# Kernel tuning notes

Hardware: AMD Instinct MI355X
Metric: run time of the kernel (lower is better)

The kernel has to match this reference:

```python
import jax, jax.numpy as jnp
import numpy as np

B, N, R, E = 4, 50000, 100000, 1_600_000   # batch, nodes (wavelets_col), wavelets_row, nnz
D_IN, H1, H2, D_OUT = 32, 32, 16, 1
NEG_SLOPE = 0.2


def _xavier(k, shape):
    lim = float(np.sqrt(6.0 / (shape[0] + shape[1])))
    return jax.random.uniform(k, shape, jnp.float32, -lim, lim)


def setup_inputs() -> dict:
    key = jax.random.key(0)
    ks = jax.random.split(key, 16)
    # wavelets: sparse (R x N); inverse wavelets: sparse (N x R)
    w_rows = jax.random.randint(ks[0], (E,), 0, R)
    w_cols = jax.random.randint(ks[1], (E,), 0, N)
    wi_rows = jax.random.randint(ks[2], (E,), 0, N)
    wi_cols = jax.random.randint(ks[3], (E,), 0, R)
    return {
        "wavelets_indices": jnp.stack([w_rows, w_cols]),
        "wavelets_values": jax.random.normal(ks[4], (E,), jnp.float32) * 0.05,
        "wavelets_inverse_indices": jnp.stack([wi_rows, wi_cols]),
        "wavelets_inverse_values": jax.random.normal(ks[5], (E,), jnp.float32) * 0.05,
        "x_features": jax.random.normal(ks[6], (B, N, D_IN), jnp.float32),
        "W1": _xavier(ks[7], (D_IN, H1)),
        "diag1": 0.9 + 0.2 * jax.random.uniform(ks[8], (R,), jnp.float32),
        "W2": _xavier(ks[9], (H1, H2)),
        "diag2": 0.9 + 0.2 * jax.random.uniform(ks[10], (R,), jnp.float32),
        "reg_co_w": _xavier(ks[11], (H2, D_OUT)),
        "reg_co_b": jnp.zeros((D_OUT,), jnp.float32),
        "reg_co2_w": _xavier(ks[12], (H2, D_OUT)),
        "reg_co2_b": jnp.zeros((D_OUT,), jnp.float32),
    }


def _gw_layer(x, W, diag, w_idx, w_val, wi_idx, wi_val):
    # filtered = X @ W  -> (B, N, d)
    h = jnp.einsum("bnd,de->bne", x, W)
    d = W.shape[1]
    # T = wavelets (R x N) @ h  : scatter-add of gathered edge messages
    msg = h[:, w_idx[1], :] * w_val[None, :, None]          # (B, E, d)
    t = jnp.zeros((x.shape[0], R, d), h.dtype).at[:, w_idx[0], :].add(msg)
    # out = (wavelets_inverse * diag) (N x R) @ T  (diag rescales columns)
    coef = wi_val * diag[wi_idx[1]]                         # (E,)
    msg2 = t[:, wi_idx[1], :] * coef[None, :, None]         # (B, E, d)
    out = jnp.zeros((x.shape[0], N, d), h.dtype).at[:, wi_idx[0], :].add(msg2)
    return jax.nn.leaky_relu(out, NEG_SLOPE)                # dropout p=0.0 -> identity


def reference(wavelets_indices, wavelets_values, wavelets_inverse_indices,
              wavelets_inverse_values, x_features, W1, diag1, W2, diag2,
              reg_co_w, reg_co_b, reg_co2_w, reg_co2_b):
    x = _gw_layer(x_features, W1, diag1, wavelets_indices, wavelets_values,
                  wavelets_inverse_indices, wavelets_inverse_values)
    x = _gw_layer(x, W2, diag2, wavelets_indices, wavelets_values,
                  wavelets_inverse_indices, wavelets_inverse_values)
    co = x[:, -2, :] @ reg_co_w + reg_co_b                  # (B, 1)
    co2 = x[:, -1, :] @ reg_co2_w + reg_co2_b               # (B, 1)
    return jnp.concatenate([co[:, None, :], co2[:, None, :]], axis=1)  # (B, 2, 1)
```

## Files before the change

### kernel.cpp

```cpp
#include <hip/hip_runtime.h>

#define NEG_SLOPE 0.2f

static const int B = 4, N = 50000, R = 100000, E = 1600000;
static const int X2_CAP = 4096;
static const int R2_CAP = 4096;
static const int N1_CAP = 4096;
static const int WDEG  = 64;
static const int WIDEG = 96;
static const int I4PB = 512;


__global__ void fusedA(const float* __restrict__ x, const float* __restrict__ W1,
                       float* __restrict__ h1,
                       const int4* __restrict__ wi_rows4, const int* __restrict__ wi_cols,
                       const float* __restrict__ wi_val,
                       int* __restrict__ flagsR, int2* __restrict__ x2list,
                       int* __restrict__ x2tail, int* __restrict__ r2list,
                       int* __restrict__ r2tail, int e4, int G1) {
    if ((int)blockIdx.x < G1) {
        __shared__ float sW[32 * 32];
        for (int i = threadIdx.x; i < 1024; i += blockDim.x) sW[i] = W1[i];
        __syncthreads();
        int id = blockIdx.x * blockDim.x + threadIdx.x;
        if (id >= N * B) return;
        int n = id >> 2, b = id & 3;
        const float* xr = x + ((size_t)b * N + n) * 32;
        float acc[32];
#pragma unroll
        for (int c = 0; c < 32; ++c) acc[c] = 0.f;
#pragma unroll
        for (int k = 0; k < 32; ++k) {
            float xv = xr[k];
#pragma unroll
            for (int c = 0; c < 32; ++c) acc[c] += xv * sW[k * 32 + c];
        }
        float* o = h1 + ((size_t)n * B + b) * 32;
#pragma unroll
        for (int c = 0; c < 32; ++c) o[c] = acc[c];
    } else {
        int blk = blockIdx.x - G1;
        int base = blk * (blockDim.x * 4) + threadIdx.x;
#pragma unroll
        for (int k = 0; k < 4; ++k) {
            int i = base + k * blockDim.x;
            if (i >= e4) continue;
            int4 r = wi_rows4[i];
            int rr[4] = {r.x, r.y, r.z, r.w};
#pragma unroll
            for (int j = 0; j < 4; ++j) {
                if (rr[j] >= N - 2) {
                    int ed = i * 4 + j;
                    int col = wi_cols[ed];
                    int old = atomicOr(&flagsR[col], 1);
                    if (!(old & 1)) {
                        int p = atomicAdd(r2tail, 1);
                        if (p < R2_CAP) r2list[p] = col;
                    }
                    int pos = atomicAdd(x2tail, 1);
                    if (pos < X2_CAP)
                        x2list[pos] = make_int2(col * 2 + (rr[j] - (N - 2)),
                                                __float_as_int(wi_val[ed]));
                }
            }
        }
    }
}

__global__ void markB(const int4* __restrict__ w_rows4, const int* __restrict__ w_cols,
                      const int* __restrict__ flagsR, int* __restrict__ flagN1,
                      int* __restrict__ n1list, int* __restrict__ n1slot,
                      int* __restrict__ n1tail, int e4) {
    __shared__ int lcount, gbase;
    __shared__ int sbuf[2048];
    if (threadIdx.x == 0) lcount = 0;
    __syncthreads();
    int lane = threadIdx.x & 63;
#pragma unroll
    for (int k = 0; k < 2; ++k) {
        int i = blockIdx.x * I4PB + k * 256 + threadIdx.x;
        int4 r = make_int4(-1, -1, -1, -1);
        if (i < e4) r = w_rows4[i];
        int rr[4] = {r.x, r.y, r.z, r.w};
#pragma unroll
        for (int j = 0; j < 4; ++j) {
            bool isnew = false;
            int c = 0;
            if (rr[j] >= 0 && flagsR[rr[j]] != 0) {
                c = w_cols[i * 4 + j];
                int old = atomicOr(&flagN1[c], 1);
                isnew = (old == 0);
            }
            unsigned long long m = __ballot(isnew);
            if (m) {
                int leader = __ffsll(m) - 1;
                int b0 = 0;
                if (lane == leader) b0 = atomicAdd(&lcount, __popcll(m));
                b0 = __shfl(b0, leader);
                if (isnew) sbuf[b0 + __popcll(m & ((1ull << lane) - 1))] = c;
            }
        }
    }
    __syncthreads();
    if (threadIdx.x == 0) gbase = atomicAdd(n1tail, lcount);
    __syncthreads();
    for (int t = threadIdx.x; t < lcount; t += blockDim.x) {
        int n = sbuf[t];
        int slot = gbase + t;
        n1list[slot] = n;
        n1slot[n] = slot;
    }
}

__global__ void markC_wi(const int4* __restrict__ wi_rows4, const int* __restrict__ wi_cols,
                         const float* __restrict__ wi_val, const float* __restrict__ diag1,
                         const int* __restrict__ flagN1, const int* __restrict__ n1slot,
                         int* __restrict__ flagsR, int* __restrict__ wi_cnt,
                         int2* __restrict__ wi_pairsD,
                         int* __restrict__ r1list, int* __restrict__ r1tail, int e4) {
    __shared__ int lcount2, gbase2;
    __shared__ int r1buf[2048];
    if (threadIdx.x == 0) lcount2 = 0;
    __syncthreads();
    int lane = threadIdx.x & 63;
#pragma unroll
    for (int k = 0; k < 2; ++k) {
        int i = blockIdx.x * I4PB + k * 256 + threadIdx.x;
        int4 r = make_int4(-1, -1, -1, -1);
        if (i < e4) r = wi_rows4[i];
        int rr[4] = {r.x, r.y, r.z, r.w};
#pragma unroll
        for (int j = 0; j < 4; ++j) {
            bool isnew = false;
            if (rr[j] >= 0 && flagN1[rr[j]] != 0) {
                int ed = i * 4 + j;
                int col = wi_cols[ed];
                float cf = wi_val[ed] * diag1[col];
                int slot = n1slot[rr[j]];
                int pos = atomicAdd(&wi_cnt[rr[j]], 1);
                if (slot < N1_CAP && pos < WIDEG)
                    wi_pairsD[(size_t)slot * WIDEG + pos] =
                        make_int2(col, __float_as_int(cf));
                int old = atomicOr(&flagsR[col], 2);
                isnew = !(old & 2);
                if (isnew) {  }
            }
            unsigned long long m2 = __ballot(isnew);
            if (m2) {
                int leader = __ffsll(m2) - 1;
                int b0 = 0;
                if (lane == leader) b0 = atomicAdd(&lcount2, __popcll(m2));
                b0 = __shfl(b0, leader);
                if (isnew)
                    r1buf[b0 + __popcll(m2 & ((1ull << lane) - 1))] =
                        wi_cols[i * 4 + j];
            }
        }
    }
    __syncthreads();
    if (threadIdx.x == 0) gbase2 = atomicAdd(r1tail, lcount2);
    __syncthreads();
    for (int t = threadIdx.x; t < lcount2; t += blockDim.x) r1list[gbase2 + t] = r1buf[t];
}

__global__ void wplace(const int4* __restrict__ w_rows4, const int* __restrict__ w_cols,
                       const float* __restrict__ w_val, const int* __restrict__ flagsR,
                       int* __restrict__ w_cnt, int2* __restrict__ w_pairsD, int e4) {
    int base = blockIdx.x * I4PB + threadIdx.x;
#pragma unroll
    for (int k = 0; k < 2; ++k) {
        int i = base + k * 256;
        if (i >= e4) continue;
        int4 r = w_rows4[i];
        int rr[4] = {r.x, r.y, r.z, r.w};
#pragma unroll
        for (int j = 0; j < 4; ++j) {
            int row = rr[j];
            if (flagsR[row] != 0) {
                int ed = i * 4 + j;
                int pos = atomicAdd(&w_cnt[row], 1);
                if (pos < WDEG)
                    w_pairsD[(size_t)row * WDEG + pos] =
                        make_int2(w_cols[ed], __float_as_int(w_val[ed]));
            }
        }
    }
}

__global__ void gather_t1(const float* __restrict__ h1, float* __restrict__ t1,
                          const int* __restrict__ w_cnt, const int2* __restrict__ w_pairsD,
                          const int* __restrict__ r1list, const int* __restrict__ r1tail) {
    int total = (*r1tail) * 32;
    int gstride = gridDim.x * blockDim.x;
    for (int idx = blockIdx.x * blockDim.x + threadIdx.x; idx < total; idx += gstride) {
        int row = r1list[idx >> 5];
        int rem = idx & 31;
        int c4 = rem & 7;
        int b = rem >> 3;
        int L = w_cnt[row]; if (L > WDEG) L = WDEG;
        const int2* pr = w_pairsD + (size_t)row * WDEG;
        const float4* sb = (const float4*)h1 + b * 8 + c4;
        float4 acc = make_float4(0.f, 0.f, 0.f, 0.f);
        int i = 0;
        int L4 = L & ~3;
        for (; i < L4; i += 4) {
            int2 p0 = pr[i + 0];
            int2 p1 = pr[i + 1];
            int2 p2 = pr[i + 2];
            int2 p3 = pr[i + 3];
            float4 s0 = sb[(size_t)p0.x * 32];
            float4 s1 = sb[(size_t)p1.x * 32];
            float4 s2 = sb[(size_t)p2.x * 32];
            float4 s3 = sb[(size_t)p3.x * 32];
            float v0 = __int_as_float(p0.y), v1 = __int_as_float(p1.y);
            float v2 = __int_as_float(p2.y), v3 = __int_as_float(p3.y);
            acc.x += v0 * s0.x + v1 * s1.x + v2 * s2.x + v3 * s3.x;
            acc.y += v0 * s0.y + v1 * s1.y + v2 * s2.y + v3 * s3.y;
            acc.z += v0 * s0.z + v1 * s1.z + v2 * s2.z + v3 * s3.z;
            acc.w += v0 * s0.w + v1 * s1.w + v2 * s2.w + v3 * s3.w;
        }
        for (; i < L; ++i) {
            int2 p = pr[i];
            float4 sv = sb[(size_t)p.x * 32];
            float v = __int_as_float(p.y);
            acc.x += v * sv.x; acc.y += v * sv.y; acc.z += v * sv.z; acc.w += v * sv.w;
        }
        ((float4*)t1)[(size_t)row * 32 + b * 8 + c4] = acc;
    }
}

__global__ void x1gemm2(const float* __restrict__ t1, const float* __restrict__ W2,
                        float* __restrict__ h2,
                        const int* __restrict__ n1list, const int* __restrict__ wi_cnt,
                        const int2* __restrict__ wi_pairsD,
                        const int* __restrict__ n1tail) {
    __shared__ float sW[32 * 16];
    __shared__ float xls[8][128];
    for (int i = threadIdx.x; i < 512; i += blockDim.x) sW[i] = W2[i];
    int n1c = *n1tail; if (n1c > N1_CAP) n1c = N1_CAP;
    int g = threadIdx.x >> 5;
    int t32 = threadIdx.x & 31;
    int b = t32 >> 3, c4 = t32 & 7;
    for (int base = blockIdx.x * 8; base < n1c; base += gridDim.x * 8) {
        int s = base + g;
        bool active = (s < n1c);
        int n = 0;
        if (active) {
            n = n1list[s];
            int L = wi_cnt[n]; if (L > WIDEG) L = WIDEG;
            const int2* pr = wi_pairsD + (size_t)s * WIDEG;
            const float4* sb = (const float4*)t1 + b * 8 + c4;
            float4 acc = make_float4(0.f, 0.f, 0.f, 0.f);
            int i = 0;
            int L2 = L & ~1;
            for (; i < L2; i += 2) {
                int2 p0 = pr[i + 0];
                int2 p1 = pr[i + 1];
                float4 s0 = sb[(size_t)p0.x * 32];
                float4 s1 = sb[(size_t)p1.x * 32];
                float v0 = __int_as_float(p0.y), v1 = __int_as_float(p1.y);
                acc.x += v0 * s0.x + v1 * s1.x;
                acc.y += v0 * s0.y + v1 * s1.y;
                acc.z += v0 * s0.z + v1 * s1.z;
                acc.w += v0 * s0.w + v1 * s1.w;
            }
            if (i < L) {
                int2 p = pr[i];
                float4 sv = sb[(size_t)p.x * 32];
                float v = __int_as_float(p.y);
                acc.x += v * sv.x; acc.y += v * sv.y; acc.z += v * sv.z; acc.w += v * sv.w;
            }
            float* xp = &xls[g][b * 32 + c4 * 4];
            xp[0] = acc.x > 0.f ? acc.x : NEG_SLOPE * acc.x;
            xp[1] = acc.y > 0.f ? acc.y : NEG_SLOPE * acc.y;
            xp[2] = acc.z > 0.f ? acc.z : NEG_SLOPE * acc.z;
            xp[3] = acc.w > 0.f ? acc.w : NEG_SLOPE * acc.w;
        }
        __syncthreads();
        if (active) {
#pragma unroll
            for (int half = 0; half < 2; ++half) {
                int o = t32 + half * 32;
                int bb = o >> 4, cc = o & 15;
                const float* xp = &xls[g][bb * 32];
                float acc = 0.f;
#pragma unroll
                for (int k = 0; k < 32; ++k) acc += xp[k] * sW[k * 16 + cc];
                h2[(size_t)n * 64 + o] = acc;
            }
        }
        __syncthreads();
    }
}

__global__ void t2x2heads(const float* __restrict__ h2,
                          const int* __restrict__ w_cnt, const int2* __restrict__ w_pairsD,
                          const int* __restrict__ n1slot,
                          const int* __restrict__ r2list, const int* __restrict__ r2tail,
                          float* __restrict__ t2,
                          const int2* __restrict__ x2list, const int* __restrict__ x2tail,
                          const float* __restrict__ diag2,
                          const float* __restrict__ rw1, const float* __restrict__ rb1,
                          const float* __restrict__ rw2, const float* __restrict__ rb2,
                          float* __restrict__ out) {
    int r2c = *r2tail; if (r2c > R2_CAP) r2c = R2_CAP;
    for (int idx = threadIdx.x; idx < r2c * 16; idx += blockDim.x) {
        int row = r2list[idx >> 4];
        int rem = idx & 15;
        int c4 = rem & 3;
        int b = rem >> 2;
        int L = w_cnt[row]; if (L > WDEG) L = WDEG;
        const int2* pr = w_pairsD + (size_t)row * WDEG;
        const float4* sb = (const float4*)h2 + b * 4 + c4;
        float4 acc = make_float4(0.f, 0.f, 0.f, 0.f);
        for (int i = 0; i < L; ++i) {
            int2 p = pr[i];
            float4 sv = sb[(size_t)p.x * 16];
            float v = __int_as_float(p.y);
            acc.x += v * sv.x; acc.y += v * sv.y; acc.z += v * sv.z; acc.w += v * sv.w;
        }
        ((float4*)t2)[(size_t)row * 16 + b * 4 + c4] = acc;
    }
    __syncthreads();

    int cnt = *x2tail; if (cnt > X2_CAP) cnt = X2_CAP;
    int g = threadIdx.x >> 6, l = threadIdx.x & 63;
    int b = l >> 4, c = l & 15;
    float a0 = 0.f, a1 = 0.f;
    for (int i = g; i < cnt; i += 16) {
        int2 rec = x2list[i];
        int col = rec.x >> 1;
        float coef = __int_as_float(rec.y) * diag2[col];
        float v = t2[(size_t)col * 64 + b * 16 + c] * coef;
        if (rec.x & 1) a1 += v; else a0 += v;
    }
    __shared__ float red0[16][64], red1[16][64], xs[2][64];
    red0[g][l] = a0; red1[g][l] = a1;
    __syncthreads();
    if (threadIdx.x < 64) {
        float s0 = 0.f, s1 = 0.f;
#pragma unroll
        for (int gg = 0; gg < 16; ++gg) { s0 += red0[gg][l]; s1 += red1[gg][l]; }
        xs[0][l] = s0; xs[1][l] = s1;
    }
    __syncthreads();
    if (threadIdx.x < 8) {
        int bb = threadIdx.x >> 1, which = threadIdx.x & 1;
        const float* w = which ? rw2 : rw1;
        float acc = which ? rb2[0] : rb1[0];
        for (int k = 0; k < 16; ++k) {
            float xv = xs[which][bb * 16 + k];
            xv = xv > 0.f ? xv : NEG_SLOPE * xv;
            acc += xv * w[k];
        }
        out[bb * 2 + which] = acc;
    }
}

extern "C" void kernel_launch(void* const* d_in, const int* in_sizes, int n_in,
                              void* d_out, int out_size, void* d_ws, size_t ws_size,
                              hipStream_t stream) {
    const int*   w_rows  = (const int*)d_in[0];
    const int*   w_cols  = ((const int*)d_in[0]) + E;
    const float* w_val   = (const float*)d_in[1];
    const int*   wi_rows = (const int*)d_in[2];
    const int*   wi_cols = ((const int*)d_in[2]) + E;
    const float* wi_val  = (const float*)d_in[3];
    const float* x       = (const float*)d_in[4];
    const float* W1      = (const float*)d_in[5];
    const float* diag1   = (const float*)d_in[6];
    const float* W2      = (const float*)d_in[7];
    const float* diag2   = (const float*)d_in[8];
    const float* rw1     = (const float*)d_in[9];
    const float* rb1     = (const float*)d_in[10];
    const float* rw2     = (const float*)d_in[11];
    const float* rb2     = (const float*)d_in[12];
    float* out = (float*)d_out;

    float* h1 = (float*)d_ws;
    float* t1 = h1 + (size_t)B * N * 32;
    float* h2 = t1 + (size_t)B * R * 32;
    int* ip = (int*)(h2 + (size_t)B * N * 16);
    int* w_cnt  = ip; ip += R;
    int* wi_cnt = ip; ip += N;
    int* flagsR = ip; ip += R;
    int* flagN1 = ip; ip += N;
    int* tails  = ip; ip += 8;
    size_t zero_words = (size_t)(ip - w_cnt);
    int*  n1slot = ip; ip += N;
    int*  n1list = ip; ip += N;
    int*  r1list = ip; ip += R;
    int*  r2list = ip; ip += R2_CAP;
    int2* x2list = (int2*)ip; ip += 2 * X2_CAP;
    int2* w_pairsD  = (int2*)ip; ip += 2 * (size_t)R * WDEG;
    int2* wi_pairsD = (int2*)ip; ip += 2 * (size_t)N1_CAP * WIDEG;

    float* t2 = t1;

    const int blk = 256;
    const int e4 = E / 4;
    const int G1 = (N * B + blk - 1) / blk;
    const int G2 = (e4 + blk * 4 - 1) / (blk * 4);
    const int stageGrid = (e4 + I4PB - 1) / I4PB;

    (void)hipMemsetAsync(w_cnt, 0, zero_words * sizeof(int), stream);

    fusedA<<<G1 + G2, blk, 0, stream>>>(x, W1, h1, (const int4*)wi_rows, wi_cols, wi_val,
                                        flagsR, x2list, tails + 0, r2list, tails + 1,
                                        e4, G1);
    markB<<<stageGrid, blk, 0, stream>>>((const int4*)w_rows, w_cols, flagsR, flagN1,
                                         n1list, n1slot, tails + 2, e4);
    markC_wi<<<stageGrid, blk, 0, stream>>>((const int4*)wi_rows, wi_cols, wi_val, diag1,
                                            flagN1, n1slot, flagsR, wi_cnt, wi_pairsD,
                                            r1list, tails + 3, e4);
    wplace<<<stageGrid, blk, 0, stream>>>((const int4*)w_rows, w_cols, w_val, flagsR,
                                          w_cnt, w_pairsD, e4);
    gather_t1<<<4096, blk, 0, stream>>>(h1, t1, w_cnt, w_pairsD, r1list, tails + 3);
    x1gemm2<<<256, blk, 0, stream>>>(t1, W2, h2, n1list, wi_cnt, wi_pairsD, tails + 2);
    t2x2heads<<<1, 1024, 0, stream>>>(h2, w_cnt, w_pairsD, n1slot, r2list, tails + 1,
                                      t2, x2list, tails + 0, diag2,
                                      rw1, rb1, rw2, rb2, out);
}
```

Measured before the change: 266.3 us.

## Build full CSR buckets once, then compute frontier in a single-block kernel

Replaces the four edge-scanning marking passes (fusedA edge part, markB, markC_wi, wplace) with one fused pass that buckets every edge of both sparse matrices by row. A single 1024-thread block then walks those buckets to derive the small backward-reachable sets (x2, r2, n1, r1) using shared-memory bitmaps, instead of rescanning all 1.6M edges per stage. The diag1 scaling moves into x1gemm2, and wi_pairsD is now indexed by node rather than slot. In exchange, atomics and writes now cover all edges instead of only the flagged ones. The frontier stage is serialised on one block, and the smaller caps (R2_CAP, X2_CAP, WIDEG) risk truncation.

Result: slower. 417.1 us (+56.6%).

```diff
diff --git a/kernel.cpp b/kernel.cpp
--- a/kernel.cpp
+++ b/kernel.cpp
@@ -3,21 +3,21 @@
 #define NEG_SLOPE 0.2f
 
 static const int B = 4, N = 50000, R = 100000, E = 1600000;
-static const int X2_CAP = 4096;
-static const int R2_CAP = 4096;
+static const int WDEG  = 64;
+static const int WIDEG = 80;
+static const int R2_CAP = 1024;
 static const int N1_CAP = 4096;
-static const int WDEG  = 64;
-static const int WIDEG = 96;
-static const int I4PB = 512;
-
-
-__global__ void fusedA(const float* __restrict__ x, const float* __restrict__ W1,
-                       float* __restrict__ h1,
-                       const int4* __restrict__ wi_rows4, const int* __restrict__ wi_cols,
-                       const float* __restrict__ wi_val,
-                       int* __restrict__ flagsR, int2* __restrict__ x2list,
-                       int* __restrict__ x2tail, int* __restrict__ r2list,
-                       int* __restrict__ r2tail, int e4, int G1) {
+static const int X2_CAP = 2048;
+
+__global__ void build_all(const float* __restrict__ x, const float* __restrict__ W1,
+                          float* __restrict__ h1,
+                          const int4* __restrict__ w_rows4, const int4* __restrict__ w_cols4,
+                          const float4* __restrict__ w_val4,
+                          const int4* __restrict__ wi_rows4, const int4* __restrict__ wi_cols4,
+                          const float4* __restrict__ wi_val4,
+                          int* __restrict__ w_cnt, int2* __restrict__ w_pairsD,
+                          int* __restrict__ wi_cnt, int2* __restrict__ wi_pairsD,
+                          int e4, int G1) {
     if ((int)blockIdx.x < G1) {
         __shared__ float sW[32 * 32];
         for (int i = threadIdx.x; i < 1024; i += blockDim.x) sW[i] = W1[i];
@@ -38,152 +38,118 @@
         float* o = h1 + ((size_t)n * B + b) * 32;
 #pragma unroll
         for (int c = 0; c < 32; ++c) o[c] = acc[c];
-    } else {
-        int blk = blockIdx.x - G1;
-        int base = blk * (blockDim.x * 4) + threadIdx.x;
-#pragma unroll
-        for (int k = 0; k < 4; ++k) {
-            int i = base + k * blockDim.x;
-            if (i >= e4) continue;
-            int4 r = wi_rows4[i];
-            int rr[4] = {r.x, r.y, r.z, r.w};
-#pragma unroll
-            for (int j = 0; j < 4; ++j) {
-                if (rr[j] >= N - 2) {
-                    int ed = i * 4 + j;
-                    int col = wi_cols[ed];
-                    int old = atomicOr(&flagsR[col], 1);
-                    if (!(old & 1)) {
-                        int p = atomicAdd(r2tail, 1);
-                        if (p < R2_CAP) r2list[p] = col;
-                    }
-                    int pos = atomicAdd(x2tail, 1);
-                    if (pos < X2_CAP)
-                        x2list[pos] = make_int2(col * 2 + (rr[j] - (N - 2)),
-                                                __float_as_int(wi_val[ed]));
-                }
-            }
-        }
-    }
-}
-
-__global__ void markB(const int4* __restrict__ w_rows4, const int* __restrict__ w_cols,
-                      const int* __restrict__ flagsR, int* __restrict__ flagN1,
-                      int* __restrict__ n1list, int* __restrict__ n1slot,
-                      int* __restrict__ n1tail, int e4) {
-    __shared__ int lcount, gbase;
-    __shared__ int sbuf[2048];
-    if (threadIdx.x == 0) lcount = 0;
-    __syncthreads();
-    int lane = threadIdx.x & 63;
+        return;
+    }
+    int blk = blockIdx.x - G1;
 #pragma unroll
     for (int k = 0; k < 2; ++k) {
-        int i = blockIdx.x * I4PB + k * 256 + threadIdx.x;
-        int4 r = make_int4(-1, -1, -1, -1);
-        if (i < e4) r = w_rows4[i];
-        int rr[4] = {r.x, r.y, r.z, r.w};
+        int i = blk * 512 + k * 256 + threadIdx.x;
+        if (i >= e4) continue;
+        int4 wr = w_rows4[i];
+        int4 wc = w_cols4[i];
+        float4 wv = w_val4[i];
+        int rr[4] = {wr.x, wr.y, wr.z, wr.w};
+        int cc[4] = {wc.x, wc.y, wc.z, wc.w};
+        float vv[4] = {wv.x, wv.y, wv.z, wv.w};
 #pragma unroll
         for (int j = 0; j < 4; ++j) {
-            bool isnew = false;
-            int c = 0;
-            if (rr[j] >= 0 && flagsR[rr[j]] != 0) {
-                c = w_cols[i * 4 + j];
-                int old = atomicOr(&flagN1[c], 1);
-                isnew = (old == 0);
-            }
-            unsigned long long m = __ballot(isnew);
-            if (m) {
-                int leader = __ffsll(m) - 1;
-                int b0 = 0;
-                if (lane == leader) b0 = atomicAdd(&lcount, __popcll(m));
-                b0 = __shfl(b0, leader);
-                if (isnew) sbuf[b0 + __popcll(m & ((1ull << lane) - 1))] = c;
-            }
-        }
-    }
-    __syncthreads();
-    if (threadIdx.x == 0) gbase = atomicAdd(n1tail, lcount);
-    __syncthreads();
-    for (int t = threadIdx.x; t < lcount; t += blockDim.x) {
-        int n = sbuf[t];
-        int slot = gbase + t;
-        n1list[slot] = n;
-        n1slot[n] = slot;
-    }
-}
-
-__global__ void markC_wi(const int4* __restrict__ wi_rows4, const int* __restrict__ wi_cols,
-                         const float* __restrict__ wi_val, const float* __restrict__ diag1,
-                         const int* __restrict__ flagN1, const int* __restrict__ n1slot,
-                         int* __restrict__ flagsR, int* __restrict__ wi_cnt,
-                         int2* __restrict__ wi_pairsD,
-                         int* __restrict__ r1list, int* __restrict__ r1tail, int e4) {
-    __shared__ int lcount2, gbase2;
-    __shared__ int r1buf[2048];
-    if (threadIdx.x == 0) lcount2 = 0;
-    __syncthreads();
-    int lane = threadIdx.x & 63;
-#pragma unroll
-    for (int k = 0; k < 2; ++k) {
-        int i = blockIdx.x * I4PB + k * 256 + threadIdx.x;
-        int4 r = make_int4(-1, -1, -1, -1);
-        if (i < e4) r = wi_rows4[i];
-        int rr[4] = {r.x, r.y, r.z, r.w};
+            int pos = atomicAdd(&w_cnt[rr[j]], 1);
+            if (pos < WDEG)
+                w_pairsD[(size_t)rr[j] * WDEG + pos] =
+                    make_int2(cc[j], __float_as_int(vv[j]));
+        }
+        int4 ir = wi_rows4[i];
+        int4 ic = wi_cols4[i];
+        float4 iv = wi_val4[i];
+        int r2[4] = {ir.x, ir.y, ir.z, ir.w};
+        int c2[4] = {ic.x, ic.y, ic.z, ic.w};
+        float v2[4] = {iv.x, iv.y, iv.z, iv.w};
 #pragma unroll
         for (int j = 0; j < 4; ++j) {
-            bool isnew = false;
-            if (rr[j] >= 0 && flagN1[rr[j]] != 0) {
-                int ed = i * 4 + j;
-                int col = wi_cols[ed];
-                float cf = wi_val[ed] * diag1[col];
-                int slot = n1slot[rr[j]];
-                int pos = atomicAdd(&wi_cnt[rr[j]], 1);
-                if (slot < N1_CAP && pos < WIDEG)
-                    wi_pairsD[(size_t)slot * WIDEG + pos] =
-                        make_int2(col, __float_as_int(cf));
-                int old = atomicOr(&flagsR[col], 2);
-                isnew = !(old & 2);
-                if (isnew) {  }
-            }
-            unsigned long long m2 = __ballot(isnew);
-            if (m2) {
-                int leader = __ffsll(m2) - 1;
-                int b0 = 0;
-                if (lane == leader) b0 = atomicAdd(&lcount2, __popcll(m2));
-                b0 = __shfl(b0, leader);
-                if (isnew)
-                    r1buf[b0 + __popcll(m2 & ((1ull << lane) - 1))] =
-                        wi_cols[i * 4 + j];
-            }
-        }
-    }
-    __syncthreads();
-    if (threadIdx.x == 0) gbase2 = atomicAdd(r1tail, lcount2);
-    __syncthreads();
-    for (int t = threadIdx.x; t < lcount2; t += blockDim.x) r1list[gbase2 + t] = r1buf[t];
-}
-
-__global__ void wplace(const int4* __restrict__ w_rows4, const int* __restrict__ w_cols,
-                       const float* __restrict__ w_val, const int* __restrict__ flagsR,
-                       int* __restrict__ w_cnt, int2* __restrict__ w_pairsD, int e4) {
-    int base = blockIdx.x * I4PB + threadIdx.x;
-#pragma unroll
-    for (int k = 0; k < 2; ++k) {
-        int i = base + k * 256;
-        if (i >= e4) continue;
-        int4 r = w_rows4[i];
-        int rr[4] = {r.x, r.y, r.z, r.w};
-#pragma unroll
-        for (int j = 0; j < 4; ++j) {
-            int row = rr[j];
-            if (flagsR[row] != 0) {
-                int ed = i * 4 + j;
-                int pos = atomicAdd(&w_cnt[row], 1);
-                if (pos < WDEG)
-                    w_pairsD[(size_t)row * WDEG + pos] =
-                        make_int2(w_cols[ed], __float_as_int(w_val[ed]));
-            }
-        }
+            int pos = atomicAdd(&wi_cnt[r2[j]], 1);
+            if (pos < WIDEG)
+                wi_pairsD[(size_t)r2[j] * WIDEG + pos] =
+                    make_int2(c2[j], __float_as_int(v2[j]));
+        }
+    }
+}
+
+__global__ __launch_bounds__(1024)
+void frontier(const int* __restrict__ w_cnt, const int2* __restrict__ w_pairsD,
+              const int* __restrict__ wi_cnt, const int2* __restrict__ wi_pairsD,
+              int2* __restrict__ x2list, int* __restrict__ r2list,
+              int* __restrict__ n1list, int* __restrict__ r1list,
+              int* __restrict__ tails ) {
+    __shared__ unsigned mR2[3128];
+    __shared__ unsigned mN1[1568];
+    __shared__ unsigned mR1[3128];
+    __shared__ int r2buf[R2_CAP];
+    __shared__ int n1buf[N1_CAP];
+    __shared__ int cx2, cr2, cn1, cr1;
+    int tid = threadIdx.x;
+    for (int i = tid; i < 3128; i += 1024) { mR2[i] = 0; mR1[i] = 0; }
+    for (int i = tid; i < 1568; i += 1024) mN1[i] = 0;
+    if (tid == 0) { cx2 = 0; cr2 = 0; cn1 = 0; cr1 = 0; }
+    __syncthreads();
+
+    for (int idx = tid; idx < 2 * WIDEG; idx += 1024) {
+        int which = idx / WIDEG;
+        int pos = idx - which * WIDEG;
+        int row = N - 2 + which;
+        int L = wi_cnt[row]; if (L > WIDEG) L = WIDEG;
+        if (pos < L) {
+            int2 p = wi_pairsD[(size_t)row * WIDEG + pos];
+            int col = p.x;
+            int q = atomicAdd(&cx2, 1);
+            if (q < X2_CAP) x2list[q] = make_int2(col * 2 + which, p.y);
+            unsigned bit = 1u << (col & 31);
+            unsigned old = atomicOr(&mR2[col >> 5], bit);
+            if (!(old & bit)) {
+                int t = atomicAdd(&cr2, 1);
+                if (t < R2_CAP) r2buf[t] = col;
+            }
+        }
+    }
+    __syncthreads();
+    int r2c = cr2; if (r2c > R2_CAP) r2c = R2_CAP;
+
+    for (int idx = tid; idx < r2c * WDEG; idx += 1024) {
+        int i = idx >> 6, pos = idx & 63;
+        int row = r2buf[i];
+        int L = w_cnt[row]; if (L > WDEG) L = WDEG;
+        if (pos < L) {
+            int col = w_pairsD[(size_t)row * WDEG + pos].x;
+            unsigned bit = 1u << (col & 31);
+            unsigned old = atomicOr(&mN1[col >> 5], bit);
+            if (!(old & bit)) {
+                int t = atomicAdd(&cn1, 1);
+                if (t < N1_CAP) n1buf[t] = col;
+            }
+        }
+    }
+    __syncthreads();
+    int n1c = cn1; if (n1c > N1_CAP) n1c = N1_CAP;
+
+    for (int idx = tid; idx < n1c * WIDEG; idx += 1024) {
+        int i = idx / WIDEG, pos = idx - i * WIDEG;
+        int n = n1buf[i];
+        int L = wi_cnt[n]; if (L > WIDEG) L = WIDEG;
+        if (pos < L) {
+            int col = wi_pairsD[(size_t)n * WIDEG + pos].x;
+            unsigned bit = 1u << (col & 31);
+            unsigned old = atomicOr(&mR1[col >> 5], bit);
+            if (!(old & bit)) {
+                int t = atomicAdd(&cr1, 1);
+                r1list[t] = col;
+            }
+        }
+    }
+    __syncthreads();
+    for (int t = tid; t < r2c; t += 1024) r2list[t] = r2buf[t];
+    for (int t = tid; t < n1c; t += 1024) n1list[t] = n1buf[t];
+    if (tid == 0) {
+        int x2c = cx2; if (x2c > X2_CAP) x2c = X2_CAP;
+        tails[0] = x2c; tails[1] = r2c; tails[2] = n1c; tails[3] = cr1;
     }
 }
 
@@ -230,7 +196,7 @@
 }
 
 __global__ void x1gemm2(const float* __restrict__ t1, const float* __restrict__ W2,
-                        float* __restrict__ h2,
+                        const float* __restrict__ diag1, float* __restrict__ h2,
                         const int* __restrict__ n1list, const int* __restrict__ wi_cnt,
                         const int2* __restrict__ wi_pairsD,
                         const int* __restrict__ n1tail) {
@@ -248,7 +214,7 @@
         if (active) {
             n = n1list[s];
             int L = wi_cnt[n]; if (L > WIDEG) L = WIDEG;
-            const int2* pr = wi_pairsD + (size_t)s * WIDEG;
+            const int2* pr = wi_pairsD + (size_t)n * WIDEG;
             const float4* sb = (const float4*)t1 + b * 8 + c4;
             float4 acc = make_float4(0.f, 0.f, 0.f, 0.f);
             int i = 0;
@@ -258,7 +224,8 @@
                 int2 p1 = pr[i + 1];
                 float4 s0 = sb[(size_t)p0.x * 32];
                 float4 s1 = sb[(size_t)p1.x * 32];
-                float v0 = __int_as_float(p0.y), v1 = __int_as_float(p1.y);
+                float v0 = __int_as_float(p0.y) * diag1[p0.x];
+                float v1 = __int_as_float(p1.y) * diag1[p1.x];
                 acc.x += v0 * s0.x + v1 * s1.x;
                 acc.y += v0 * s0.y + v1 * s1.y;
                 acc.z += v0 * s0.z + v1 * s1.z;
@@ -267,7 +234,7 @@
             if (i < L) {
                 int2 p = pr[i];
                 float4 sv = sb[(size_t)p.x * 32];
-                float v = __int_as_float(p.y);
+                float v = __int_as_float(p.y) * diag1[p.x];
                 acc.x += v * sv.x; acc.y += v * sv.y; acc.z += v * sv.z; acc.w += v * sv.w;
             }
             float* xp = &xls[g][b * 32 + c4 * 4];
@@ -295,7 +262,6 @@
 
 __global__ void t2x2heads(const float* __restrict__ h2,
                           const int* __restrict__ w_cnt, const int2* __restrict__ w_pairsD,
-                          const int* __restrict__ n1slot,
                           const int* __restrict__ r2list, const int* __restrict__ r2tail,
                           float* __restrict__ t2,
                           const int2* __restrict__ x2list, const int* __restrict__ x2tail,
@@ -383,41 +349,39 @@
     int* ip = (int*)(h2 + (size_t)B * N * 16);
     int* w_cnt  = ip; ip += R;
     int* wi_cnt = ip; ip += N;
-    int* flagsR = ip; ip += R;
-    int* flagN1 = ip; ip += N;
+    size_t zero_words = (size_t)(ip - w_cnt);
     int* tails  = ip; ip += 8;
-    size_t zero_words = (size_t)(ip - w_cnt);
-    int*  n1slot = ip; ip += N;
-    int*  n1list = ip; ip += N;
-    int*  r1list = ip; ip += R;
-    int*  r2list = ip; ip += R2_CAP;
+    int* r2list = ip; ip += R2_CAP;
+    int* n1list = ip; ip += N1_CAP;
+    int* r1list = ip; ip += R;
     int2* x2list = (int2*)ip; ip += 2 * X2_CAP;
     int2* w_pairsD  = (int2*)ip; ip += 2 * (size_t)R * WDEG;
-    int2* wi_pairsD = (int2*)ip; ip += 2 * (size_t)N1_CAP * WIDEG;
+    int2* wi_pairsD = (int2*)ip; ip += 2 * (size_t)N * WIDEG;
 
     float* t2 = t1;
 
     const int blk = 256;
     const int e4 = E / 4;
     const int G1 = (N * B + blk - 1) / blk;
-    const int G2 = (e4 + blk * 4 - 1) / (blk * 4);
-    const int stageGrid = (e4 + I4PB - 1) / I4PB;
+    const int Gs = (e4 + 511) / 512;
 
     (void)hipMemsetAsync(w_cnt, 0, zero_words * sizeof(int), stream);
 
-    fusedA<<<G1 + G2, blk, 0, stream>>>(x, W1, h1, (const int4*)wi_rows, wi_cols, wi_val,
-                                        flagsR, x2list, tails + 0, r2list, tails + 1,
-                                        e4, G1);
-    markB<<<stageGrid, blk, 0, stream>>>((const int4*)w_rows, w_cols, flagsR, flagN1,
-                                         n1list, n1slot, tails + 2, e4);
-    markC_wi<<<stageGrid, blk, 0, stream>>>((const int4*)wi_rows, wi_cols, wi_val, diag1,
-                                            flagN1, n1slot, flagsR, wi_cnt, wi_pairsD,
-                                            r1list, tails + 3, e4);
-    wplace<<<stageGrid, blk, 0, stream>>>((const int4*)w_rows, w_cols, w_val, flagsR,
-                                          w_cnt, w_pairsD, e4);
+    build_all<<<G1 + Gs, blk, 0, stream>>>(
+        x, W1, h1,
+        (const int4*)w_rows, (const int4*)w_cols, (const float4*)w_val,
+        (const int4*)wi_rows, (const int4*)wi_cols, (const float4*)wi_val,
+        w_cnt, w_pairsD, wi_cnt, wi_pairsD, e4, G1);
+
+    frontier<<<1, 1024, 0, stream>>>(w_cnt, w_pairsD, wi_cnt, wi_pairsD,
+                                     x2list, r2list, n1list, r1list, tails);
+
     gather_t1<<<4096, blk, 0, stream>>>(h1, t1, w_cnt, w_pairsD, r1list, tails + 3);
-    x1gemm2<<<256, blk, 0, stream>>>(t1, W2, h2, n1list, wi_cnt, wi_pairsD, tails + 2);
-    t2x2heads<<<1, 1024, 0, stream>>>(h2, w_cnt, w_pairsD, n1slot, r2list, tails + 1,
+
+    x1gemm2<<<256, blk, 0, stream>>>(t1, W2, diag1, h2, n1list, wi_cnt, wi_pairsD,
+                                     tails + 2);
+
+    t2x2heads<<<1, 1024, 0, stream>>>(h2, w_cnt, w_pairsD, r2list, tails + 1,
                                       t2, x2list, tails + 0, diag2,
                                       rw1, rb1, rw2, rb2, out);
 }
```

## Fuse layer-1 T gather into per-node x1 computation, dropping r1list and t1

Applied to the files above, without the earlier changes.

Removes the separate gather_t1 pass and the t1 buffer. The new fused kernel has each needed layer-2 input node recompute its wavelet rows on the fly from h1, accumulating across four sub-groups and reducing in shared memory before the W2 projection. markC_wi no longer compacts an r1 row list. This removes the t1 write/read traffic and one launch, but rows shared by several nodes are now computed redundantly. Caps on the r2/x2 lists are also lowered.

After: 292.0 us. +9.6%, slower.

```diff
diff --git a/kernel.cpp b/kernel.cpp
--- a/kernel.cpp
+++ b/kernel.cpp
@@ -3,11 +3,11 @@
 #define NEG_SLOPE 0.2f
 
 static const int B = 4, N = 50000, R = 100000, E = 1600000;
-static const int X2_CAP = 4096;
-static const int R2_CAP = 4096;
-static const int N1_CAP = 4096;
 static const int WDEG  = 64;
 static const int WIDEG = 96;
+static const int R2_CAP = 1024;
+static const int N1_CAP = 4096;
+static const int X2_CAP = 2048;
 static const int I4PB = 512;
 
 
@@ -107,8 +107,7 @@
     for (int t = threadIdx.x; t < lcount; t += blockDim.x) {
         int n = sbuf[t];
         int slot = gbase + t;
-        n1list[slot] = n;
-        n1slot[n] = slot;
+        if (slot < N1_CAP) { n1list[slot] = n; n1slot[n] = slot; }
     }
 }
 
@@ -116,51 +115,30 @@
                          const float* __restrict__ wi_val, const float* __restrict__ diag1,
                          const int* __restrict__ flagN1, const int* __restrict__ n1slot,
                          int* __restrict__ flagsR, int* __restrict__ wi_cnt,
-                         int2* __restrict__ wi_pairsD,
-                         int* __restrict__ r1list, int* __restrict__ r1tail, int e4) {
-    __shared__ int lcount2, gbase2;
-    __shared__ int r1buf[2048];
-    if (threadIdx.x == 0) lcount2 = 0;
-    __syncthreads();
-    int lane = threadIdx.x & 63;
+                         int2* __restrict__ wi_pairsD, int e4) {
+    int base = blockIdx.x * I4PB + threadIdx.x;
 #pragma unroll
     for (int k = 0; k < 2; ++k) {
-        int i = blockIdx.x * I4PB + k * 256 + threadIdx.x;
-        int4 r = make_int4(-1, -1, -1, -1);
-        if (i < e4) r = wi_rows4[i];
+        int i = base + k * 256;
+        if (i >= e4) continue;
+        int4 r = wi_rows4[i];
         int rr[4] = {r.x, r.y, r.z, r.w};
 #pragma unroll
         for (int j = 0; j < 4; ++j) {
-            bool isnew = false;
-            if (rr[j] >= 0 && flagN1[rr[j]] != 0) {
+            int row = rr[j];
+            if (flagN1[row] != 0) {
                 int ed = i * 4 + j;
                 int col = wi_cols[ed];
                 float cf = wi_val[ed] * diag1[col];
-                int slot = n1slot[rr[j]];
-                int pos = atomicAdd(&wi_cnt[rr[j]], 1);
+                int slot = n1slot[row];
+                int pos = atomicAdd(&wi_cnt[row], 1);
                 if (slot < N1_CAP && pos < WIDEG)
                     wi_pairsD[(size_t)slot * WIDEG + pos] =
                         make_int2(col, __float_as_int(cf));
-                int old = atomicOr(&flagsR[col], 2);
-                isnew = !(old & 2);
-                if (isnew) {  }
-            }
-            unsigned long long m2 = __ballot(isnew);
-            if (m2) {
-                int leader = __ffsll(m2) - 1;
-                int b0 = 0;
-                if (lane == leader) b0 = atomicAdd(&lcount2, __popcll(m2));
-                b0 = __shfl(b0, leader);
-                if (isnew)
-                    r1buf[b0 + __popcll(m2 & ((1ull << lane) - 1))] =
-                        wi_cols[i * 4 + j];
-            }
-        }
-    }
-    __syncthreads();
-    if (threadIdx.x == 0) gbase2 = atomicAdd(r1tail, lcount2);
-    __syncthreads();
-    for (int t = threadIdx.x; t < lcount2; t += blockDim.x) r1list[gbase2 + t] = r1buf[t];
+                atomicOr(&flagsR[col], 2);
+            }
+        }
+    }
 }
 
 __global__ void wplace(const int4* __restrict__ w_rows4, const int* __restrict__ w_cols,
@@ -187,107 +165,76 @@
     }
 }
 
-__global__ void gather_t1(const float* __restrict__ h1, float* __restrict__ t1,
-                          const int* __restrict__ w_cnt, const int2* __restrict__ w_pairsD,
-                          const int* __restrict__ r1list, const int* __restrict__ r1tail) {
-    int total = (*r1tail) * 32;
-    int gstride = gridDim.x * blockDim.x;
-    for (int idx = blockIdx.x * blockDim.x + threadIdx.x; idx < total; idx += gstride) {
-        int row = r1list[idx >> 5];
-        int rem = idx & 31;
-        int c4 = rem & 7;
-        int b = rem >> 3;
-        int L = w_cnt[row]; if (L > WDEG) L = WDEG;
-        const int2* pr = w_pairsD + (size_t)row * WDEG;
-        const float4* sb = (const float4*)h1 + b * 8 + c4;
-        float4 acc = make_float4(0.f, 0.f, 0.f, 0.f);
-        int i = 0;
-        int L4 = L & ~3;
-        for (; i < L4; i += 4) {
-            int2 p0 = pr[i + 0];
-            int2 p1 = pr[i + 1];
-            int2 p2 = pr[i + 2];
-            int2 p3 = pr[i + 3];
-            float4 s0 = sb[(size_t)p0.x * 32];
-            float4 s1 = sb[(size_t)p1.x * 32];
-            float4 s2 = sb[(size_t)p2.x * 32];
-            float4 s3 = sb[(size_t)p3.x * 32];
-            float v0 = __int_as_float(p0.y), v1 = __int_as_float(p1.y);
-            float v2 = __int_as_float(p2.y), v3 = __int_as_float(p3.y);
-            acc.x += v0 * s0.x + v1 * s1.x + v2 * s2.x + v3 * s3.x;
-            acc.y += v0 * s0.y + v1 * s1.y + v2 * s2.y + v3 * s3.y;
-            acc.z += v0 * s0.z + v1 * s1.z + v2 * s2.z + v3 * s3.z;
-            acc.w += v0 * s0.w + v1 * s1.w + v2 * s2.w + v3 * s3.w;
-        }
-        for (; i < L; ++i) {
-            int2 p = pr[i];
-            float4 sv = sb[(size_t)p.x * 32];
-            float v = __int_as_float(p.y);
-            acc.x += v * sv.x; acc.y += v * sv.y; acc.z += v * sv.z; acc.w += v * sv.w;
-        }
-        ((float4*)t1)[(size_t)row * 32 + b * 8 + c4] = acc;
-    }
-}
-
-__global__ void x1gemm2(const float* __restrict__ t1, const float* __restrict__ W2,
-                        float* __restrict__ h2,
-                        const int* __restrict__ n1list, const int* __restrict__ wi_cnt,
-                        const int2* __restrict__ wi_pairsD,
-                        const int* __restrict__ n1tail) {
-    __shared__ float sW[32 * 16];
-    __shared__ float xls[8][128];
-    for (int i = threadIdx.x; i < 512; i += blockDim.x) sW[i] = W2[i];
+__global__ __launch_bounds__(256)
+void x1fused(const float* __restrict__ h1, const float* __restrict__ W2,
+             float* __restrict__ h2,
+             const int* __restrict__ n1list, const int* __restrict__ wi_cnt,
+             const int2* __restrict__ wi_pairsD,
+             const int* __restrict__ w_cnt, const int2* __restrict__ w_pairsD,
+             const int* __restrict__ n1tail) {
+    __shared__ float sW[512];
+    __shared__ float xpart[2][4][128];
+    for (int i = threadIdx.x; i < 512; i += 256) sW[i] = W2[i];
     int n1c = *n1tail; if (n1c > N1_CAP) n1c = N1_CAP;
-    int g = threadIdx.x >> 5;
+    int g2 = threadIdx.x >> 7;
+    int sub = (threadIdx.x >> 5) & 3;
     int t32 = threadIdx.x & 31;
     int b = t32 >> 3, c4 = t32 & 7;
-    for (int base = blockIdx.x * 8; base < n1c; base += gridDim.x * 8) {
-        int s = base + g;
+    __syncthreads();
+    for (int base = blockIdx.x * 2; base < n1c; base += gridDim.x * 2) {
+        int s = base + g2;
         bool active = (s < n1c);
         int n = 0;
+        float4 acc = make_float4(0.f, 0.f, 0.f, 0.f);
         if (active) {
             n = n1list[s];
             int L = wi_cnt[n]; if (L > WIDEG) L = WIDEG;
             const int2* pr = wi_pairsD + (size_t)s * WIDEG;
-            const float4* sb = (const float4*)t1 + b * 8 + c4;
-            float4 acc = make_float4(0.f, 0.f, 0.f, 0.f);
-            int i = 0;
-            int L2 = L & ~1;
-            for (; i < L2; i += 2) {
-                int2 p0 = pr[i + 0];
-                int2 p1 = pr[i + 1];
-                float4 s0 = sb[(size_t)p0.x * 32];
-                float4 s1 = sb[(size_t)p1.x * 32];
-                float v0 = __int_as_float(p0.y), v1 = __int_as_float(p1.y);
-                acc.x += v0 * s0.x + v1 * s1.x;
-                acc.y += v0 * s0.y + v1 * s1.y;
-                acc.z += v0 * s0.z + v1 * s1.z;
-                acc.w += v0 * s0.w + v1 * s1.w;
-            }
-            if (i < L) {
-                int2 p = pr[i];
-                float4 sv = sb[(size_t)p.x * 32];
-                float v = __int_as_float(p.y);
-                acc.x += v * sv.x; acc.y += v * sv.y; acc.z += v * sv.z; acc.w += v * sv.w;
-            }
-            float* xp = &xls[g][b * 32 + c4 * 4];
-            xp[0] = acc.x > 0.f ? acc.x : NEG_SLOPE * acc.x;
-            xp[1] = acc.y > 0.f ? acc.y : NEG_SLOPE * acc.y;
-            xp[2] = acc.z > 0.f ? acc.z : NEG_SLOPE * acc.z;
-            xp[3] = acc.w > 0.f ? acc.w : NEG_SLOPE * acc.w;
-        }
+            const float4* hb = (const float4*)h1 + b * 8 + c4;
+            for (int e = sub; e < L; e += 4) {
+                int2 p = pr[e];
+                float cf = __int_as_float(p.y);
+                int col = p.x;
+                int Lw = w_cnt[col]; if (Lw > WDEG) Lw = WDEG;
+                const int2* pw = w_pairsD + (size_t)col * WDEG;
+                float4 t = make_float4(0.f, 0.f, 0.f, 0.f);
+                int i = 0;
+                int Lw2 = Lw & ~1;
+                for (; i < Lw2; i += 2) {
+                    int2 q0 = pw[i], q1 = pw[i + 1];
+                    float4 s0 = hb[(size_t)q0.x * 32];
+                    float4 s1 = hb[(size_t)q1.x * 32];
+                    float v0 = __int_as_float(q0.y), v1 = __int_as_float(q1.y);
+                    t.x += v0 * s0.x + v1 * s1.x;
+                    t.y += v0 * s0.y + v1 * s1.y;
+                    t.z += v0 * s0.z + v1 * s1.z;
+                    t.w += v0 * s0.w + v1 * s1.w;
+                }
+                if (i < Lw) {
+                    int2 q = pw[i];
+                    float4 s0 = hb[(size_t)q.x * 32];
+                    float v = __int_as_float(q.y);
+                    t.x += v * s0.x; t.y += v * s0.y; t.z += v * s0.z; t.w += v * s0.w;
+                }
+                acc.x += cf * t.x; acc.y += cf * t.y;
+                acc.z += cf * t.z; acc.w += cf * t.w;
+            }
+        }
+        float* xp = &xpart[g2][sub][b * 32 + c4 * 4];
+        xp[0] = acc.x; xp[1] = acc.y; xp[2] = acc.z; xp[3] = acc.w;
         __syncthreads();
-        if (active) {
-#pragma unroll
-            for (int half = 0; half < 2; ++half) {
-                int o = t32 + half * 32;
-                int bb = o >> 4, cc = o & 15;
-                const float* xp = &xls[g][bb * 32];
-                float acc = 0.f;
-#pragma unroll
-                for (int k = 0; k < 32; ++k) acc += xp[k] * sW[k * 16 + cc];
-                h2[(size_t)n * 64 + o] = acc;
-            }
+        int tid128 = threadIdx.x & 127;
+        if (active && tid128 < 64) {
+            int bb = tid128 >> 4, cc = tid128 & 15;
+            float accum = 0.f;
+#pragma unroll
+            for (int k = 0; k < 32; ++k) {
+                float xv = xpart[g2][0][bb * 32 + k] + xpart[g2][1][bb * 32 + k]
+                         + xpart[g2][2][bb * 32 + k] + xpart[g2][3][bb * 32 + k];
+                xv = xv > 0.f ? xv : NEG_SLOPE * xv;
+                accum += xv * sW[k * 16 + cc];
+            }
+            h2[(size_t)n * 64 + tid128] = accum;
         }
         __syncthreads();
     }
@@ -295,7 +242,6 @@
 
 __global__ void t2x2heads(const float* __restrict__ h2,
                           const int* __restrict__ w_cnt, const int2* __restrict__ w_pairsD,
-                          const int* __restrict__ n1slot,
                           const int* __restrict__ r2list, const int* __restrict__ r2tail,
                           float* __restrict__ t2,
                           const int2* __restrict__ x2list, const int* __restrict__ x2tail,
@@ -378,24 +324,21 @@
     float* out = (float*)d_out;
 
     float* h1 = (float*)d_ws;
-    float* t1 = h1 + (size_t)B * N * 32;
-    float* h2 = t1 + (size_t)B * R * 32;
-    int* ip = (int*)(h2 + (size_t)B * N * 16);
+    float* h2 = h1 + (size_t)B * N * 32;
+    float* t2 = h2 + (size_t)N * 64;
+    int* ip = (int*)(t2 + (size_t)R * 64);
     int* w_cnt  = ip; ip += R;
     int* wi_cnt = ip; ip += N;
     int* flagsR = ip; ip += R;
     int* flagN1 = ip; ip += N;
     int* tails  = ip; ip += 8;
     size_t zero_words = (size_t)(ip - w_cnt);
-    int*  n1slot = ip; ip += N;
-    int*  n1list = ip; ip += N;
-    int*  r1list = ip; ip += R;
-    int*  r2list = ip; ip += R2_CAP;
+    int* n1slot = ip; ip += N;
+    int* n1list = ip; ip += N1_CAP;
+    int* r2list = ip; ip += R2_CAP;
     int2* x2list = (int2*)ip; ip += 2 * X2_CAP;
     int2* w_pairsD  = (int2*)ip; ip += 2 * (size_t)R * WDEG;
     int2* wi_pairsD = (int2*)ip; ip += 2 * (size_t)N1_CAP * WIDEG;
-
-    float* t2 = t1;
 
     const int blk = 256;
     const int e4 = E / 4;
@@ -411,13 +354,12 @@
     markB<<<stageGrid, blk, 0, stream>>>((const int4*)w_rows, w_cols, flagsR, flagN1,
                                          n1list, n1slot, tails + 2, e4);
     markC_wi<<<stageGrid, blk, 0, stream>>>((const int4*)wi_rows, wi_cols, wi_val, diag1,
-                                            flagN1, n1slot, flagsR, wi_cnt, wi_pairsD,
-                                            r1list, tails + 3, e4);
+                                            flagN1, n1slot, flagsR, wi_cnt, wi_pairsD, e4);
     wplace<<<stageGrid, blk, 0, stream>>>((const int4*)w_rows, w_cols, w_val, flagsR,
                                           w_cnt, w_pairsD, e4);
-    gather_t1<<<4096, blk, 0, stream>>>(h1, t1, w_cnt, w_pairsD, r1list, tails + 3);
-    x1gemm2<<<256, blk, 0, stream>>>(t1, W2, h2, n1list, wi_cnt, wi_pairsD, tails + 2);
-    t2x2heads<<<1, 1024, 0, stream>>>(h2, w_cnt, w_pairsD, n1slot, r2list, tails + 1,
+    x1fused<<<512, blk, 0, stream>>>(h1, W2, h2, n1list, wi_cnt, wi_pairsD,
+                                     w_cnt, w_pairsD, tails + 2);
+    t2x2heads<<<1, 1024, 0, stream>>>(h2, w_cnt, w_pairsD, r2list, tails + 1,
                                       t2, x2list, tails + 0, diag2,
                                       rw1, rb1, rw2, rb2, out);
 }
```
